# Kernel tuning notes

Measured on AMD Instinct MI355X. Metric: run time of the kernel, lower is better.

Reference implementation:

```python
import jax, jax.numpy as jnp
import numpy as np

N = 100000
E = 1600000
IN = 128
HID = 128
OUT = 64


def sage_conv(x, src, dst, deg_inv, W_l, b_l, W_r):
    # PyG SAGEConv (mean aggr): out = lin_l(mean_{j in N(i)} x_j) + lin_r(x_i)
    msgs = x[src]                                   # [E, F] gather
    agg = jax.ops.segment_sum(msgs, dst, num_segments=N)  # [N, F]
    agg = agg * deg_inv[:, None]                    # mean
    return agg @ W_l + b_l + x @ W_r


def setup_inputs() -> dict:
    key = jax.random.key(0)
    ks = jax.random.split(key, 9)
    x = jax.random.normal(ks[0], (N, IN), dtype=jnp.float32)
    edge_index = jax.random.randint(ks[1], (2, E), 0, N, dtype=jnp.int64)
    s = 1.0 / np.sqrt(IN)
    W1l = jax.random.uniform(ks[2], (IN, HID), jnp.float32, -s, s)
    b1 = jax.random.uniform(ks[3], (HID,), jnp.float32, -s, s)
    W1r = jax.random.uniform(ks[4], (IN, HID), jnp.float32, -s, s)
    s2 = 1.0 / np.sqrt(HID)
    W2l = jax.random.uniform(ks[5], (HID, HID), jnp.float32, -s2, s2)
    b2 = jax.random.uniform(ks[6], (HID,), jnp.float32, -s2, s2)
    W2r = jax.random.uniform(ks[7], (HID, HID), jnp.float32, -s2, s2)
    kl1, kl2 = jax.random.split(ks[8])
    Wlin = jax.random.uniform(kl1, (HID, OUT), jnp.float32, -s2, s2)
    blin = jax.random.uniform(kl2, (OUT,), jnp.float32, -s2, s2)
    return {"x": x, "edge_index": edge_index, "W1l": W1l, "b1": b1, "W1r": W1r,
            "W2l": W2l, "b2": b2, "W2r": W2r, "Wlin": Wlin, "blin": blin}


def reference(x, edge_index, W1l, b1, W1r, W2l, b2, W2r, Wlin, blin):
    src, dst = edge_index[0], edge_index[1]
    deg = jax.ops.segment_sum(jnp.ones((E,), jnp.float32), dst, num_segments=N)
    deg_inv = 1.0 / jnp.maximum(deg, 1.0)
    h = sage_conv(x, src, dst, deg_inv, W1l, b1, W1r)
    h = jax.nn.relu(h)
    # dropout: training=False -> identity
    h2 = sage_conv(h, src, dst, deg_inv, W2l, b2, W2r)
    h = jax.nn.relu(h + h2)
    return h @ Wlin + blin
```

## Files before the change

### kernel.cpp

```cpp
#include <hip/hip_runtime.h>
#include <hip/hip_bf16.h>
#include <cstdint>

#define NND 100000
#define NED 1600000
#define FIN 128
#define FOUT 64

#define NBLK 512
#define EPB (NED / NBLK)
#define NBUCK 256
#define BSH 9
#define BNODES 512
#define HTN (NBUCK * NBLK)

#define NSLICE 4
#define NPW 8
#define AGGB_BLK (NSLICE * (NND / (NPW * 4)))
#define EMAX 512

typedef __bf16 bf16x8 __attribute__((ext_vector_type(8)));
typedef float f32x4 __attribute__((ext_vector_type(4)));

static __device__ inline unsigned short f2bf(float f) {
    unsigned int u = __builtin_bit_cast(unsigned int, f);
    unsigned int r = (u + 0x7fffu + ((u >> 16) & 1u)) >> 16;
    return (unsigned short)r;
}
static __device__ inline float bflo(unsigned int v) {
    return __builtin_bit_cast(float, v << 16);
}
static __device__ inline float bfhi(unsigned int v) {
    return __builtin_bit_cast(float, v & 0xffff0000u);
}
static __device__ inline float bf1(unsigned short u) {
    return __builtin_bit_cast(float, (unsigned int)u << 16);
}

static __device__ inline void pack_one(const float* __restrict__ W,
                                       unsigned short* __restrict__ out,
                                       int NTtot, int c_local, int nt,
                                       int chunkOff, int ncols, int lane) {
    int k = c_local * 32 + (lane >> 4) * 8;
    int n = nt * 16 + (lane & 15);
    unsigned short t[8];
#pragma unroll
    for (int j = 0; j < 8; j++) t[j] = f2bf(W[(size_t)(k + j) * ncols + n]);
    uint4 u;
    u.x = t[0] | ((unsigned)t[1] << 16);
    u.y = t[2] | ((unsigned)t[3] << 16);
    u.z = t[4] | ((unsigned)t[5] << 16);
    u.w = t[6] | ((unsigned)t[7] << 16);
    *(uint4*)&out[((size_t)((c_local + chunkOff) * NTtot + nt) * 64 + lane) * 8] = u;
}

__global__ __launch_bounds__(256) void k_hist_cast(
        const int* __restrict__ dst, int* __restrict__ histT,
        const float* __restrict__ x, unsigned int* __restrict__ xb,
        const float* W1l, const float* W1r, const float* W2l,
        const float* W2r, const float* Wlin,
        unsigned short* p1, unsigned short* p2, unsigned short* ph) {
    __shared__ int hist[NBUCK];
    const int tid = threadIdx.x, blk = blockIdx.x;
    hist[tid] = 0;
    __syncthreads();
    const int e0 = blk * EPB, e1 = e0 + EPB;
    for (int i = e0 + tid; i < e1; i += 256)
        atomicAdd(&hist[dst[i] >> BSH], 1);
    __syncthreads();
    histT[tid * NBLK + blk] = hist[tid];
    if (blk < 144 && tid < 64) {
        int b = blk, lane = tid;
        if (b < 32)       pack_one(W1l, p1, 8, b >> 3, b & 7, 0, 128, lane);
        else if (b < 64)  { b -= 32; pack_one(W1r, p1, 8, b >> 3, b & 7, 4, 128, lane); }
        else if (b < 96)  { b -= 64; pack_one(W2l, p2, 8, b >> 3, b & 7, 0, 128, lane); }
        else if (b < 128) { b -= 96; pack_one(W2r, p2, 8, b >> 3, b & 7, 4, 128, lane); }
        else              { b -= 128; pack_one(Wlin, ph, 4, b >> 2, b & 3, 0, 64, lane); }
    }
    const int total = NND * 32;
    for (int i = blk * 256 + tid; i < total; i += NBLK * 256) {
        int node = i >> 5;
        int c4 = i & 31;
        float4 v = ((const float4*)x)[i];
        uint2 o;
        o.x = (unsigned)f2bf(v.x) | ((unsigned)f2bf(v.y) << 16);
        o.y = (unsigned)f2bf(v.z) | ((unsigned)f2bf(v.w) << 16);
        int s = c4 >> 3;
        int part = c4 & 7;
        ((uint2*)xb)[((size_t)s * NND + node) * 8 + part] = o;
    }
}

__global__ __launch_bounds__(1024) void g_scan1(const int* __restrict__ in,
                                                int* __restrict__ psum, int n) {
    __shared__ int red[1024];
    int tid = threadIdx.x;
    int i = blockIdx.x * 1024 + tid;
    red[tid] = (i < n) ? in[i] : 0;
    __syncthreads();
#pragma unroll
    for (int off = 512; off > 0; off >>= 1) {
        if (tid < off) red[tid] += red[tid + off];
        __syncthreads();
    }
    if (tid == 0) psum[blockIdx.x] = red[0];
}

__global__ __launch_bounds__(128) void g_scan2(int* __restrict__ psum, int nb) {
    int tid = threadIdx.x;
    int d = (tid < nb) ? psum[tid] : 0;
    int v = d;
#pragma unroll
    for (int off = 1; off < 64; off <<= 1) {
        int u = __shfl_up(v, off, 64);
        if ((tid & 63) >= off) v += u;
    }
    __shared__ int ws[2];
    if ((tid & 63) == 63) ws[tid >> 6] = v;
    __syncthreads();
    int base = (tid >= 64) ? ws[0] : 0;
    if (tid < nb) psum[tid] = base + v - d;
}

__global__ __launch_bounds__(1024) void g_scan3(const int* __restrict__ in,
                                                const int* __restrict__ psum,
                                                int* __restrict__ out, int n) {
    int tid = threadIdx.x;
    int i = blockIdx.x * 1024 + tid;
    int d = (i < n) ? in[i] : 0;
    int v = d;
#pragma unroll
    for (int off = 1; off < 64; off <<= 1) {
        int u = __shfl_up(v, off, 64);
        if ((tid & 63) >= off) v += u;
    }
    __shared__ int wsum[16];
    int wid = tid >> 6;
    if ((tid & 63) == 63) wsum[wid] = v;
    __syncthreads();
    if (tid < 16) {
        int w = wsum[tid];
#pragma unroll
        for (int off = 1; off < 16; off <<= 1) {
            int u = __shfl_up(w, off, 64);
            if (tid >= off) w += u;
        }
        wsum[tid] = w;
    }
    __syncthreads();
    int base = psum[blockIdx.x] + (wid ? wsum[wid - 1] : 0);
    if (i < n) out[i] = base + v - d;
}

__global__ __launch_bounds__(256) void k_scatter(const int* __restrict__ src,
                                                 const int* __restrict__ dst,
                                                 const int* __restrict__ sh,
                                                 unsigned int* __restrict__ eS) {
    __shared__ int cur[NBUCK];
    const int tid = threadIdx.x, blk = blockIdx.x;
    cur[tid] = sh[tid * NBLK + blk];
    __syncthreads();
    const int e0 = blk * EPB, e1 = e0 + EPB;
    for (int i = e0 + tid; i < e1; i += 256) {
        int d = dst[i];
        int pos = atomicAdd(&cur[d >> BSH], 1);
        eS[pos] = (unsigned)src[i] | ((unsigned)(d & (BNODES - 1)) << 17);
    }
}

__global__ __launch_bounds__(1024) void k_bucket(const unsigned int* __restrict__ eS,
                                                 const int* __restrict__ sh,
                                                 int* __restrict__ csr,
                                                 int* __restrict__ offs,
                                                 float* __restrict__ dinv, int n) {
    __shared__ int cnt[BNODES];
    __shared__ int loc[BNODES];
    const int b = blockIdx.x, tid = threadIdx.x;
    const int base = sh[b * NBLK];
    const int end = (b == NBUCK - 1) ? NED : sh[(b + 1) * NBLK];
    if (tid < BNODES) cnt[tid] = 0;
    __syncthreads();
    for (int i = base + tid; i < end; i += 1024)
        atomicAdd(&cnt[eS[i] >> 17], 1);
    __syncthreads();
    if (tid < BNODES) loc[tid] = cnt[tid];
    __syncthreads();
#pragma unroll
    for (int off = 1; off < BNODES; off <<= 1) {
        int v = 0;
        if (tid < BNODES && tid >= off) v = loc[tid - off];
        __syncthreads();
        if (tid < BNODES) loc[tid] += v;
        __syncthreads();
    }
    int node = b * BNODES + tid;
    int myExcl = 0;
    if (tid < BNODES) {
        myExcl = loc[tid] - cnt[tid];
        if (node < n) {
            offs[node] = base + myExcl;
            dinv[node] = 1.0f / fmaxf((float)cnt[tid], 1.0f);
        }
    }
    __syncthreads();
    if (tid < BNODES) cnt[tid] = base + myExcl;
    __syncthreads();
    for (int i = base + tid; i < end; i += 1024) {
        unsigned int e = eS[i];
        int slot = atomicAdd(&cnt[e >> 17], 1);
        csr[slot] = (int)(e & 0x1FFFFu);
    }
    if (b == 0 && tid == 0) offs[n] = NED;
}

#define ACC2(v) do { \
    acc.x += bflo((v).x); acc.y += bfhi((v).x); \
    acc.z += bflo((v).y); acc.w += bfhi((v).y); } while (0)

__global__ __launch_bounds__(256) void k_aggb(const unsigned short* __restrict__ featS,
                                              const int* __restrict__ offs,
                                              const int* __restrict__ csr,
                                              const float* __restrict__ dinv,
                                              unsigned short* __restrict__ outS, int n) {
    __shared__ int eids[4][EMAX];
    const int s = blockIdx.x & 3;
    const int wv = threadIdx.x >> 6;
    const int wslot = (blockIdx.x >> 2) * 4 + wv;
    const int lane = threadIdx.x & 63;
    const int g = lane >> 3;
    const int q = lane & 7;
    const uint2* fS = (const uint2*)featS + (size_t)s * n * 8;
    uint2* oS = (uint2*)outS + (size_t)s * n * 8;

    const int base = wslot * NPW;
    const int node = base + g;
    const bool valid = node < n;
    const int nc = valid ? node : n - 1;
    const int beg = offs[nc];
    const int end = offs[nc + 1];
    const int begW = __shfl(beg, 0);
    const int endW = __shfl(end, 63);
    const int lim = min(endW - begW, EMAX);
    for (int i = lane; i < lim; i += 64)
        eids[wv][i] = csr[begW + i];
    __syncthreads();

    f32x4 acc = (f32x4){0.f, 0.f, 0.f, 0.f};
    const int deg = valid ? (end - beg) : 0;
    const int lb = beg - begW;

    int j = 0;
    for (; j + 8 <= deg; j += 8) {
        int i0, i1, i2, i3, i4, i5, i6, i7;
        if (lb + j + 8 <= EMAX) {
            i0 = eids[wv][lb + j];     i1 = eids[wv][lb + j + 1];
            i2 = eids[wv][lb + j + 2]; i3 = eids[wv][lb + j + 3];
            i4 = eids[wv][lb + j + 4]; i5 = eids[wv][lb + j + 5];
            i6 = eids[wv][lb + j + 6]; i7 = eids[wv][lb + j + 7];
        } else {
            i0 = csr[beg + j];     i1 = csr[beg + j + 1];
            i2 = csr[beg + j + 2]; i3 = csr[beg + j + 3];
            i4 = csr[beg + j + 4]; i5 = csr[beg + j + 5];
            i6 = csr[beg + j + 6]; i7 = csr[beg + j + 7];
        }
        uint2 v0 = fS[(unsigned)i0 * 8u + q];
        uint2 v1 = fS[(unsigned)i1 * 8u + q];
        uint2 v2 = fS[(unsigned)i2 * 8u + q];
        uint2 v3 = fS[(unsigned)i3 * 8u + q];
        uint2 v4 = fS[(unsigned)i4 * 8u + q];
        uint2 v5 = fS[(unsigned)i5 * 8u + q];
        uint2 v6 = fS[(unsigned)i6 * 8u + q];
        uint2 v7 = fS[(unsigned)i7 * 8u + q];
        ACC2(v0); ACC2(v1); ACC2(v2); ACC2(v3);
        ACC2(v4); ACC2(v5); ACC2(v6); ACC2(v7);
    }
    {
        uint2 t0 = make_uint2(0u, 0u), t1 = t0, t2 = t0, t3 = t0;
        uint2 t4 = t0, t5 = t0, t6 = t0, t7 = t0;
#define TAIL(K, TV) do { \
        if (j + K < deg) { \
            int li = lb + j + K; \
            int id = (li < EMAX) ? eids[wv][li] : csr[beg + j + K]; \
            TV = fS[(unsigned)id * 8u + q]; \
        } } while (0)
        TAIL(0, t0); TAIL(1, t1); TAIL(2, t2); TAIL(3, t3);
        TAIL(4, t4); TAIL(5, t5); TAIL(6, t6); TAIL(7, t7);
#undef TAIL
        ACC2(t0); ACC2(t1); ACC2(t2); ACC2(t3);
        ACC2(t4); ACC2(t5); ACC2(t6); ACC2(t7);
    }

    if (valid) {
        float di = dinv[node];
        uint2 o;
        o.x = (unsigned)f2bf(acc.x * di) | ((unsigned)f2bf(acc.y * di) << 16);
        o.y = (unsigned)f2bf(acc.z * di) | ((unsigned)f2bf(acc.w * di) << 16);
        oS[(size_t)node * 8 + q] = o;
    }
}

template <int NT, int KCH, bool TWO, bool RELU, bool RESID, bool HEAD, bool OUTBF>
__global__ __launch_bounds__(256) void k_mfma(const unsigned short* __restrict__ P,
                                              const unsigned short* __restrict__ Q,
                                              const unsigned short* __restrict__ Wp,
                                              const float* __restrict__ bias,
                                              const unsigned short* __restrict__ resid,
                                              const unsigned short* __restrict__ Wp2,
                                              const float* __restrict__ bias2,
                                              void* __restrict__ outv, int n) {
    const int lane = threadIdx.x & 63;
    const int wave = threadIdx.x >> 6;
    const int quad = lane >> 4;
    const int row0 = blockIdx.x * 64 + wave * 16;
    int rowA = row0 + (lane & 15);
    if (rowA >= n) rowA = n - 1;

    f32x4 acc[NT];
#pragma unroll
    for (int t = 0; t < NT; t++) acc[t] = (f32x4){0.f, 0.f, 0.f, 0.f};

#pragma unroll
    for (int c = 0; c < KCH; c++) {
        const unsigned short* Abase = (TWO && c >= KCH / 2) ? Q : P;
        const int kk = (TWO ? (c & (KCH / 2 - 1)) : c) * 32 + quad * 8;
        bf16x8 a = *(const bf16x8*)&Abase[((size_t)(kk >> 5) * NND + rowA) * 32 + (kk & 31)];
#pragma unroll
        for (int t = 0; t < NT; t++) {
            bf16x8 b = *(const bf16x8*)&Wp[(size_t)((c * NT + t) * 64 + lane) * 8];
            acc[t] = __builtin_amdgcn_mfma_f32_16x16x32_bf16(a, b, acc[t], 0, 0, 0);
        }
    }

    const int col = lane & 15;
    if (!HEAD) {
#pragma unroll
        for (int t = 0; t < NT; t++) {
            float bv = bias[t * 16 + col];
#pragma unroll
            for (int r = 0; r < 4; r++) {
                int row = row0 + quad * 4 + r;
                if (row < n) {
                    float v = acc[t][r] + bv;
                    if (RESID) v += bf1(resid[((size_t)(t >> 1) * NND + row) * 32 + (t & 1) * 16 + col]);
                    if (RELU) v = fmaxf(v, 0.f);
                    if (OUTBF)
                        ((unsigned short*)outv)[((size_t)(t >> 1) * NND + row) * 32 + (t & 1) * 16 + col] = f2bf(v);
                    else
                        ((float*)outv)[(size_t)row * (NT * 16) + t * 16 + col] = v;
                }
            }
        }
    } else {
        __shared__ __align__(16) unsigned short sT[4][16 * 136];
#pragma unroll
        for (int t = 0; t < NT; t++) {
            float bv = bias[t * 16 + col];
#pragma unroll
            for (int r = 0; r < 4; r++) {
                int row = row0 + quad * 4 + r;
                int rr = row < n ? row : n - 1;
                float v = acc[t][r] + bv;
                if (RESID) v += bf1(resid[((size_t)(t >> 1) * NND + rr) * 32 + (t & 1) * 16 + col]);
                if (RELU) v = fmaxf(v, 0.f);
                sT[wave][(quad * 4 + r) * 136 + t * 16 + col] = f2bf(v);
            }
        }
        f32x4 hacc[4];
#pragma unroll
        for (int t = 0; t < 4; t++) hacc[t] = (f32x4){0.f, 0.f, 0.f, 0.f};
#pragma unroll
        for (int c = 0; c < 4; c++) {
            bf16x8 a = *(const bf16x8*)&sT[wave][(lane & 15) * 136 + c * 32 + quad * 8];
#pragma unroll
            for (int t = 0; t < 4; t++) {
                bf16x8 b = *(const bf16x8*)&Wp2[(size_t)((c * 4 + t) * 64 + lane) * 8];
                hacc[t] = __builtin_amdgcn_mfma_f32_16x16x32_bf16(a, b, hacc[t], 0, 0, 0);
            }
        }
#pragma unroll
        for (int t = 0; t < 4; t++) {
            float bv = bias2[t * 16 + col];
#pragma unroll
            for (int r = 0; r < 4; r++) {
                int row = row0 + quad * 4 + r;
                if (row < n)
                    ((float*)outv)[(size_t)row * 64 + t * 16 + col] = hacc[t][r] + bv;
            }
        }
    }
}

extern "C" void kernel_launch(void* const* d_in, const int* in_sizes, int n_in,
                              void* d_out, int out_size, void* d_ws, size_t ws_size,
                              hipStream_t stream) {
    const float* x    = (const float*)d_in[0];
    const int*   ei   = (const int*)d_in[1];
    const float* W1l  = (const float*)d_in[2];
    const float* b1   = (const float*)d_in[3];
    const float* W1r  = (const float*)d_in[4];
    const float* W2l  = (const float*)d_in[5];
    const float* b2   = (const float*)d_in[6];
    const float* W2r  = (const float*)d_in[7];
    const float* Wlin = (const float*)d_in[8];
    const float* blin = (const float*)d_in[9];
    float* out = (float*)d_out;

    const int N = NND, E = NED;
    const int* src = ei;
    const int* dst = ei + E;
    const int NB2 = HTN / 1024;

    char* w = (char*)d_ws;
    int*   histT  = (int*)w;               w += (size_t)HTN * 4;
    int*   sh     = (int*)w;               w += (size_t)HTN * 4;
    int*   psum   = (int*)w;               w += (size_t)NB2 * 4;
    int*   offs   = (int*)w;               w += (size_t)(N + 4) * 4;
    float* dinv   = (float*)w;             w += (size_t)N * 4;
    unsigned int* eS = (unsigned int*)w;   w += (size_t)E * 4;
    int*   csr    = (int*)w;               w += (size_t)E * 4;
    unsigned short* p1  = (unsigned short*)w;  w += 256 * 128 * 2;
    unsigned short* p2  = (unsigned short*)w;  w += 256 * 128 * 2;
    unsigned short* ph  = (unsigned short*)w;  w += 128 * 64 * 2;
    unsigned short* xb  = (unsigned short*)w;  w += (size_t)N * 128 * 2;
    unsigned short* agg = (unsigned short*)w;  w += (size_t)N * 128 * 2;
    unsigned short* h1  = (unsigned short*)w;  w += (size_t)N * 128 * 2;

    k_hist_cast<<<NBLK, 256, 0, stream>>>(dst, histT, x, (unsigned int*)xb,
                                          W1l, W1r, W2l, W2r, Wlin, p1, p2, ph);
    g_scan1<<<NB2, 1024, 0, stream>>>(histT, psum, HTN);
    g_scan2<<<1, 128, 0, stream>>>(psum, NB2);
    g_scan3<<<NB2, 1024, 0, stream>>>(histT, psum, sh, HTN);
    k_scatter<<<NBLK, 256, 0, stream>>>(src, dst, sh, eS);
    k_bucket<<<NBUCK, 1024, 0, stream>>>(eS, sh, csr, offs, dinv, N);

    k_aggb<<<AGGB_BLK, 256, 0, stream>>>(xb, offs, csr, dinv, agg, N);
    k_mfma<8, 8, true, true, false, false, true><<<(N + 63) / 64, 256, 0, stream>>>(
        agg, xb, p1, b1, nullptr, nullptr, nullptr, h1, N);

    k_aggb<<<AGGB_BLK, 256, 0, stream>>>(h1, offs, csr, dinv, agg, N);
    k_mfma<8, 8, true, true, true, true, false><<<(N + 63) / 64, 256, 0, stream>>>(
        agg, h1, p2, b2, h1, ph, blin, out, N);
}
```

Before: 383.6 us.

## Split MFMA GEMM across waves by output columns instead of rows

Restructures the dense GEMM kernel so each wave computes all 64 rows of the block for its own 32 output columns, rather than 16 rows by all 128 columns. Each wave now loads only its slice of the packed weight matrix, cutting per-wave weight traffic, while the A fragments are read by all four waves. In the head variant the bf16 intermediate tile is shared through LDS with a __syncthreads before the final projection, since every wave needs all columns. This adds a block barrier and redundant A loads across waves.

```diff
diff --git a/kernel.cpp b/kernel.cpp
--- a/kernel.cpp
+++ b/kernel.cpp
@@ -299,7 +299,7 @@
     }
 }
 
-template <int NT, int KCH, bool TWO, bool RELU, bool RESID, bool HEAD, bool OUTBF>
+template <bool HEAD>
 __global__ __launch_bounds__(256) void k_mfma(const unsigned short* __restrict__ P,
                                               const unsigned short* __restrict__ Q,
                                               const unsigned short* __restrict__ Wp,
@@ -308,69 +308,77 @@
                                               const unsigned short* __restrict__ Wp2,
                                               const float* __restrict__ bias2,
                                               void* __restrict__ outv, int n) {
+    __shared__ __align__(16) unsigned short sT[HEAD ? 64 * 136 : 8];
     const int lane = threadIdx.x & 63;
-    const int wave = threadIdx.x >> 6;
+    const int wv = threadIdx.x >> 6;
     const int quad = lane >> 4;
-    const int row0 = blockIdx.x * 64 + wave * 16;
-    int rowA = row0 + (lane & 15);
-    if (rowA >= n) rowA = n - 1;
-
-    f32x4 acc[NT];
-#pragma unroll
-    for (int t = 0; t < NT; t++) acc[t] = (f32x4){0.f, 0.f, 0.f, 0.f};
-
-#pragma unroll
-    for (int c = 0; c < KCH; c++) {
-        const unsigned short* Abase = (TWO && c >= KCH / 2) ? Q : P;
-        const int kk = (TWO ? (c & (KCH / 2 - 1)) : c) * 32 + quad * 8;
-        bf16x8 a = *(const bf16x8*)&Abase[((size_t)(kk >> 5) * NND + rowA) * 32 + (kk & 31)];
-#pragma unroll
-        for (int t = 0; t < NT; t++) {
-            bf16x8 b = *(const bf16x8*)&Wp[(size_t)((c * NT + t) * 64 + lane) * 8];
-            acc[t] = __builtin_amdgcn_mfma_f32_16x16x32_bf16(a, b, acc[t], 0, 0, 0);
-        }
-    }
-
     const int col = lane & 15;
+    const int row0 = blockIdx.x * 64;
+
+    f32x4 acc[4][2];
+#pragma unroll
+    for (int sub = 0; sub < 4; sub++) {
+        acc[sub][0] = (f32x4){0.f, 0.f, 0.f, 0.f};
+        acc[sub][1] = (f32x4){0.f, 0.f, 0.f, 0.f};
+    }
+
+#pragma unroll
+    for (int c = 0; c < 8; c++) {
+        const unsigned short* Abase = (c >= 4) ? Q : P;
+        const int sl = c & 3;
+        const int ko = quad * 8;
+        bf16x8 b0 = *(const bf16x8*)&Wp[(size_t)((c * 8 + wv * 2 + 0) * 64 + lane) * 8];
+        bf16x8 b1 = *(const bf16x8*)&Wp[(size_t)((c * 8 + wv * 2 + 1) * 64 + lane) * 8];
+#pragma unroll
+        for (int sub = 0; sub < 4; sub++) {
+            int rowA = row0 + sub * 16 + col;
+            if (rowA >= n) rowA = n - 1;
+            bf16x8 a = *(const bf16x8*)&Abase[((size_t)sl * NND + rowA) * 32 + ko];
+            acc[sub][0] = __builtin_amdgcn_mfma_f32_16x16x32_bf16(a, b0, acc[sub][0], 0, 0, 0);
+            acc[sub][1] = __builtin_amdgcn_mfma_f32_16x16x32_bf16(a, b1, acc[sub][1], 0, 0, 0);
+        }
+    }
+
     if (!HEAD) {
 #pragma unroll
-        for (int t = 0; t < NT; t++) {
-            float bv = bias[t * 16 + col];
-#pragma unroll
-            for (int r = 0; r < 4; r++) {
-                int row = row0 + quad * 4 + r;
-                if (row < n) {
-                    float v = acc[t][r] + bv;
-                    if (RESID) v += bf1(resid[((size_t)(t >> 1) * NND + row) * 32 + (t & 1) * 16 + col]);
-                    if (RELU) v = fmaxf(v, 0.f);
-                    if (OUTBF)
-                        ((unsigned short*)outv)[((size_t)(t >> 1) * NND + row) * 32 + (t & 1) * 16 + col] = f2bf(v);
-                    else
-                        ((float*)outv)[(size_t)row * (NT * 16) + t * 16 + col] = v;
+        for (int t = 0; t < 2; t++) {
+            float bv = bias[wv * 32 + t * 16 + col];
+#pragma unroll
+            for (int sub = 0; sub < 4; sub++) {
+#pragma unroll
+                for (int r = 0; r < 4; r++) {
+                    int row = row0 + sub * 16 + quad * 4 + r;
+                    if (row < n) {
+                        float v = fmaxf(acc[sub][t][r] + bv, 0.f);
+                        ((unsigned short*)outv)[((size_t)wv * NND + row) * 32 + t * 16 + col] = f2bf(v);
+                    }
                 }
             }
         }
     } else {
-        __shared__ __align__(16) unsigned short sT[4][16 * 136];
-#pragma unroll
-        for (int t = 0; t < NT; t++) {
-            float bv = bias[t * 16 + col];
-#pragma unroll
-            for (int r = 0; r < 4; r++) {
-                int row = row0 + quad * 4 + r;
-                int rr = row < n ? row : n - 1;
-                float v = acc[t][r] + bv;
-                if (RESID) v += bf1(resid[((size_t)(t >> 1) * NND + rr) * 32 + (t & 1) * 16 + col]);
-                if (RELU) v = fmaxf(v, 0.f);
-                sT[wave][(quad * 4 + r) * 136 + t * 16 + col] = f2bf(v);
+#pragma unroll
+        for (int t = 0; t < 2; t++) {
+            float bv = bias[wv * 32 + t * 16 + col];
+#pragma unroll
+            for (int sub = 0; sub < 4; sub++) {
+#pragma unroll
+                for (int r = 0; r < 4; r++) {
+                    int row = row0 + sub * 16 + quad * 4 + r;
+                    int rr = row < n ? row : n - 1;
+                    float v = acc[sub][t][r] + bv +
+                              bf1(resid[((size_t)wv * NND + rr) * 32 + t * 16 + col]);
+                    v = fmaxf(v, 0.f);
+                    sT[(sub * 16 + quad * 4 + r) * 136 + wv * 32 + t * 16 + col] = f2bf(v);
+                }
             }
         }
+        __syncthreads();
         f32x4 hacc[4];
 #pragma unroll
         for (int t = 0; t < 4; t++) hacc[t] = (f32x4){0.f, 0.f, 0.f, 0.f};
 #pragma unroll
         for (int c = 0; c < 4; c++) {
-            bf16x8 a = *(const bf16x8*)&sT[wave][(lane & 15) * 136 + c * 32 + quad * 8];
+            bf16x8 a = *(const bf16x8*)&sT[(wv * 16 + col) * 136 + c * 32 + quad * 8];
 #pragma unroll
             for (int t = 0; t < 4; t++) {
                 bf16x8 b = *(const bf16x8*)&Wp2[(size_t)((c * 4 + t) * 64 + lane) * 8];
@@ -382,7 +390,7 @@
             float bv = bias2[t * 16 + col];
 #pragma unroll
             for (int r = 0; r < 4; r++) {
-                int row = row0 + quad * 4 + r;
+                int row = row0 + wv * 16 + quad * 4 + r;
                 if (row < n)
                     ((float*)outv)[(size_t)row * 64 + t * 16 + col] = hacc[t][r] + bv;
             }
@@ -434,10 +442,10 @@
     k_bucket<<<NBUCK, 1024, 0, stream>>>(eS, sh, csr, offs, dinv, N);
 
     k_aggb<<<AGGB_BLK, 256, 0, stream>>>(xb, offs, csr, dinv, agg, N);
-    k_mfma<8, 8, true, true, false, false, true><<<(N + 63) / 64, 256, 0, stream>>>(
+    k_mfma<false><<<(N + 63) / 64, 256, 0, stream>>>(
         agg, xb, p1, b1, nullptr, nullptr, nullptr, h1, N);
 
     k_aggb<<<AGGB_BLK, 256, 0, stream>>>(h1, offs, csr, dinv, agg, N);
-    k_mfma<8, 8, true, true, true, true, false><<<(N + 63) / 64, 256, 0, stream>>>(
+    k_mfma<true><<<(N + 63) / 64, 256, 0, stream>>>(
         agg, h1, p2, b2, h1, ph, blin, out, N);
 }
```

After: 383.6 us. No clear change (-0.0%).
